# Optimization experiments

Measured on AMD Instinct MI355X. Metric: run time of the kernel, lower is better.

## Reference

```python
import jax, jax.numpy as jnp
import numpy as np

BN_EPS = 1e-5

def _l2norm(x, axis):
    return x / (1e-6 + jnp.linalg.norm(x, axis=axis, keepdims=True))

def setup_inputs() -> dict:
    key = jax.random.key(0)
    ks = jax.random.split(key, 4)
    c, k = 512, 64
    b, h, w = 16, 64, 64
    x = jax.random.normal(ks[0], (b, c, h, w), dtype=jnp.float32)
    conv1_w = jax.random.normal(ks[1], (c, c), dtype=jnp.float32) * np.sqrt(2.0 / c)
    conv1_b = jnp.zeros((c,), dtype=jnp.float32)
    mu = jax.random.normal(ks[2], (1, c, k), dtype=jnp.float32) * np.sqrt(2.0 / k)
    mu = _l2norm(mu, axis=1)
    conv2_w = jax.random.normal(ks[3], (c, c), dtype=jnp.float32) * np.sqrt(2.0 / c)
    bn_gamma = jnp.ones((c,), dtype=jnp.float32)
    bn_beta = jnp.zeros((c,), dtype=jnp.float32)
    bn_mean = jnp.zeros((c,), dtype=jnp.float32)
    bn_var = jnp.ones((c,), dtype=jnp.float32)
    return {"x": x, "conv1_w": conv1_w, "conv1_b": conv1_b, "mu": mu,
            "conv2_w": conv2_w, "bn_gamma": bn_gamma, "bn_beta": bn_beta,
            "bn_mean": bn_mean, "bn_var": bn_var}

STAGE_NUM = 3

def reference(x, conv1_w, conv1_b, mu, conv2_w, bn_gamma, bn_beta, bn_mean, bn_var):
    idn = x
    b, c, h, w = x.shape
    # conv1: 1x1 conv with bias
    xf = jnp.einsum('oc,bchw->bohw', conv1_w, x) + conv1_b[None, :, None, None]
    xf = xf.reshape(b, c, h * w)            # [b, c, n]
    mu_b = jnp.broadcast_to(mu, (b,) + mu.shape[1:])  # [b, c, k]

    # EM iterations (no-grad in original; here just the forward loop)
    def em_step(mu_b, _):
        z = jnp.einsum('bcn,bck->bnk', xf, mu_b)          # [b, n, k]
        z = jax.nn.softmax(z, axis=2)
        z_ = z / (1e-6 + z.sum(axis=1, keepdims=True))
        mu_new = _l2norm(jnp.einsum('bcn,bnk->bck', xf, z_), axis=1)
        return mu_new, z

    mu_b, zs = jax.lax.scan(em_step, mu_b, None, length=STAGE_NUM)
    z = zs[-1]                                            # last-stage responsibilities
    mu_b = jax.lax.stop_gradient(mu_b)
    z = jax.lax.stop_gradient(z)

    xr = jnp.einsum('bck,bnk->bcn', mu_b, z).reshape(b, c, h, w)
    xr = jax.nn.relu(xr)
    # conv2: 1x1 conv (no bias) + BatchNorm (inference mode)
    xr = jnp.einsum('oc,bchw->bohw', conv2_w, xr)
    inv = bn_gamma / jnp.sqrt(bn_var + BN_EPS)
    xr = xr * inv[None, :, None, None] + (bn_beta - bn_mean * inv)[None, :, None, None]
    return jax.nn.relu(xr + idn)
```

## Files before the change

kernel.cpp:

```cpp
#include <hip/hip_runtime.h>

typedef __bf16 bf16x8 __attribute__((ext_vector_type(8)));
typedef float f32x4 __attribute__((ext_vector_type(4)));

constexpr int CC = 512;
constexpr int KK = 64;
constexpr int NN = 4096;
constexpr int BB = 16;

constexpr size_t R1_OFF    = 0;
constexpr size_t R2_OFF    = 16777216;
constexpr size_t Z_OFF     = 33554432;
constexpr size_t ZT_OFF    = 35651584;
constexpr size_t MUACC_OFF = 37748736;
constexpr size_t ZSUM_OFF  = 38273024;
constexpr size_t MUBF_OFF  = 38274048;
constexpr size_t MUTBF_OFF = 38536192;
constexpr size_t W1BF_OFF  = 38798336;
constexpr size_t W2BF_OFF  = 38929408;

__global__ __launch_bounds__(256) void k_cvt(const float* __restrict__ src,
                                             __bf16* __restrict__ dst, int n8) {
    int i = blockIdx.x * 256 + threadIdx.x;
    if (i < n8) {
        const float4* s4 = (const float4*)src;
        float4 a = s4[i * 2], b = s4[i * 2 + 1];
        bf16x8 o;
        o[0] = (__bf16)a.x; o[1] = (__bf16)a.y; o[2] = (__bf16)a.z; o[3] = (__bf16)a.w;
        o[4] = (__bf16)b.x; o[5] = (__bf16)b.y; o[6] = (__bf16)b.z; o[7] = (__bf16)b.w;
        *(bf16x8*)&dst[(size_t)i * 8] = o;
    }
}

__global__ __launch_bounds__(256) void k_mu_bcast_bf(const float* __restrict__ mu_in,
                                                     __bf16* __restrict__ mu_bf,
                                                     __bf16* __restrict__ muT_bf) {
    int idx = blockIdx.x * 256 + threadIdx.x;
    if (idx < CC * KK) {
        int c = idx >> 6, k = idx & 63;
        __bf16 v = (__bf16)mu_in[idx];
        for (int b = 0; b < BB; ++b) {
            mu_bf[(size_t)b * CC * KK + idx] = v;
            muT_bf[((size_t)b * KK + k) * CC + c] = v;
        }
    }
}

__global__ __launch_bounds__(256) void k_xpose_cvt(const float* __restrict__ X,
                                                   __bf16* __restrict__ XT) {
    int n0 = blockIdx.x * 64, c0 = blockIdx.y * 64, b = blockIdx.z;
    __shared__ float T[64][65];
    int tid = threadIdx.x;
    const float* Xb = X + (size_t)b * CC * NN;
#pragma unroll
    for (int p = 0; p < 4; ++p) {
        int f4 = tid + p * 256;
        int row = f4 >> 4, col4 = (f4 & 15) * 4;
        float4 v = *(const float4*)&Xb[(size_t)(c0 + row) * NN + n0 + col4];
        T[row][col4 + 0] = v.x; T[row][col4 + 1] = v.y;
        T[row][col4 + 2] = v.z; T[row][col4 + 3] = v.w;
    }
    __syncthreads();
#pragma unroll
    for (int p = 0; p < 2; ++p) {
        int q = tid + p * 256;
        int nl = q >> 3, c8 = (q & 7) * 8;
        bf16x8 o;
#pragma unroll
        for (int j = 0; j < 8; ++j) o[j] = (__bf16)T[c8 + j][nl];
        *(bf16x8*)&XT[((size_t)b * NN + n0 + nl) * CC + c0 + c8] = o;
    }
}

__global__ __launch_bounds__(256) void k_xftrans(const __bf16* __restrict__ XFT,
                                                 __bf16* __restrict__ XFC) {
    int n0 = blockIdx.x * 64, c0 = blockIdx.y * 64, b = blockIdx.z;
    __shared__ __bf16 T[64][66];
    int tid = threadIdx.x;
#pragma unroll
    for (int p = 0; p < 2; ++p) {
        int idx = tid + p * 256;
        int row = idx >> 3, c8 = (idx & 7) * 8;
        bf16x8 v = *(const bf16x8*)&XFT[((size_t)b * NN + n0 + row) * CC + c0 + c8];
#pragma unroll
        for (int j = 0; j < 8; ++j) T[row][c8 + j] = v[j];
    }
    __syncthreads();
#pragma unroll
    for (int p = 0; p < 2; ++p) {
        int idx = tid + p * 256;
        int crow = idx >> 3, n8 = (idx & 7) * 8;
        bf16x8 o;
#pragma unroll
        for (int j = 0; j < 8; ++j) o[j] = T[n8 + j][crow];
        *(bf16x8*)&XFC[((size_t)b * CC + c0 + crow) * NN + n0 + n8] = o;
    }
}

__global__ __launch_bounds__(256) void k_conv1_mfma(
    const __bf16* __restrict__ XT, const __bf16* __restrict__ W1,
    const float* __restrict__ bias, __bf16* __restrict__ XFT) {
    __shared__ __bf16 As[2][128 * 32];
    __shared__ __bf16 Bs[2][128 * 32];
    __shared__ float sbias[128];
    int tid = threadIdx.x;
    int lane = tid & 63, wave = tid >> 6;
    int wm = wave >> 1, wn = wave & 1;
    int o0 = blockIdx.x * 128, n0 = blockIdx.y * 128, b = blockIdx.z;
    const __bf16* Ab = XT + ((size_t)b * NN + n0) * CC;
    const __bf16* Bb = W1 + (size_t)o0 * CC;
    if (tid < 128) sbias[tid] = bias[o0 + tid];

    f32x4 acc[4][4];
#pragma unroll
    for (int i = 0; i < 4; ++i)
#pragma unroll
        for (int j = 0; j < 4; ++j) acc[i][j] = f32x4{0.f, 0.f, 0.f, 0.f};

    int r0 = tid >> 2, k0c = tid & 3;
    int r1 = (tid + 256) >> 2, k1c = tid & 3;
    int w0 = r0 * 32 + (k0c ^ ((r0 >> 1) & 3)) * 8;
    int w1 = r1 * 32 + (k1c ^ ((r1 >> 1) & 3)) * 8;

    bf16x8 va0, va1, vb0, vb1;
    va0 = *(const bf16x8*)(Ab + (size_t)r0 * CC + k0c * 8);
    va1 = *(const bf16x8*)(Ab + (size_t)r1 * CC + k1c * 8);
    vb0 = *(const bf16x8*)(Bb + (size_t)r0 * CC + k0c * 8);
    vb1 = *(const bf16x8*)(Bb + (size_t)r1 * CC + k1c * 8);
    *(bf16x8*)&As[0][w0] = va0; *(bf16x8*)&As[0][w1] = va1;
    *(bf16x8*)&Bs[0][w0] = vb0; *(bf16x8*)&Bs[0][w1] = vb1;
    __syncthreads();

    for (int kt = 0; kt < 16; ++kt) {
        int s = kt & 1;
        if (kt < 15) {
            const __bf16* Ak = Ab + (kt + 1) * 32;
            const __bf16* Bk = Bb + (kt + 1) * 32;
            va0 = *(const bf16x8*)(Ak + (size_t)r0 * CC + k0c * 8);
            va1 = *(const bf16x8*)(Ak + (size_t)r1 * CC + k1c * 8);
            vb0 = *(const bf16x8*)(Bk + (size_t)r0 * CC + k0c * 8);
            vb1 = *(const bf16x8*)(Bk + (size_t)r1 * CC + k1c * 8);
        }
        bf16x8 af[4], bg[4];
#pragma unroll
        for (int f = 0; f < 4; ++f) {
            int ra = wm * 64 + f * 16 + (lane & 15);
            af[f] = *(const bf16x8*)&As[s][ra * 32 + (((lane >> 4) ^ ((ra >> 1) & 3))) * 8];
            int rb = wn * 64 + f * 16 + (lane & 15);
            bg[f] = *(const bf16x8*)&Bs[s][rb * 32 + (((lane >> 4) ^ ((rb >> 1) & 3))) * 8];
        }
#pragma unroll
        for (int i = 0; i < 4; ++i)
#pragma unroll
            for (int j = 0; j < 4; ++j)
                acc[i][j] = __builtin_amdgcn_mfma_f32_16x16x32_bf16(af[i], bg[j], acc[i][j], 0, 0, 0);
        if (kt < 15) {
            *(bf16x8*)&As[s ^ 1][w0] = va0; *(bf16x8*)&As[s ^ 1][w1] = va1;
            *(bf16x8*)&Bs[s ^ 1][w0] = vb0; *(bf16x8*)&Bs[s ^ 1][w1] = vb1;
        }
        __syncthreads();
    }

    int gq = lane >> 4, ln = lane & 15;
#pragma unroll
    for (int mf = 0; mf < 4; ++mf) {
#pragma unroll
        for (int r = 0; r < 4; ++r) {
            int n_loc = wm * 64 + mf * 16 + gq * 4 + r;
            size_t orow = ((size_t)b * NN + n0 + n_loc) * CC + o0 + wn * 64;
#pragma unroll
            for (int nf = 0; nf < 4; ++nf) {
                int o_loc = wn * 64 + nf * 16 + ln;
                XFT[orow + nf * 16 + ln] = (__bf16)(acc[mf][nf][r] + sbias[o_loc]);
            }
        }
    }
}

__global__ __launch_bounds__(256) void k_conv2_mfma(
    const __bf16* __restrict__ A, const __bf16* __restrict__ Bt,
    const float* __restrict__ gamma, const float* __restrict__ beta,
    const float* __restrict__ mean, const float* __restrict__ var,
    const float* __restrict__ Xres, float* __restrict__ Out) {
    __shared__ __bf16 As[2][128 * 32];
    __shared__ __bf16 Bs[2][128 * 32];
    __shared__ float sp0[128], sp1[128];
    int tid = threadIdx.x;
    int lane = tid & 63, wave = tid >> 6;
    int wm = wave >> 1, wn = wave & 1;
    int n0 = blockIdx.x * 128, m0 = blockIdx.y * 128, b = blockIdx.z;
    const __bf16* Ab = A + (size_t)m0 * CC;
    const __bf16* Bb = Bt + ((size_t)b * NN + n0) * CC;
    if (tid < 128) {
        float iv = gamma[m0 + tid] * rsqrtf(var[m0 + tid] + 1e-5f);
        sp0[tid] = iv;
        sp1[tid] = beta[m0 + tid] - mean[m0 + tid] * iv;
    }

    f32x4 acc[4][4];
#pragma unroll
    for (int i = 0; i < 4; ++i)
#pragma unroll
        for (int j = 0; j < 4; ++j) acc[i][j] = f32x4{0.f, 0.f, 0.f, 0.f};

    int r0 = tid >> 2, k0c = tid & 3;
    int r1 = (tid + 256) >> 2, k1c = tid & 3;
    int w0 = r0 * 32 + (k0c ^ ((r0 >> 1) & 3)) * 8;
    int w1 = r1 * 32 + (k1c ^ ((r1 >> 1) & 3)) * 8;

    bf16x8 va0, va1, vb0, vb1;
    va0 = *(const bf16x8*)(Ab + (size_t)r0 * CC + k0c * 8);
    va1 = *(const bf16x8*)(Ab + (size_t)r1 * CC + k1c * 8);
    vb0 = *(const bf16x8*)(Bb + (size_t)r0 * CC + k0c * 8);
    vb1 = *(const bf16x8*)(Bb + (size_t)r1 * CC + k1c * 8);
    *(bf16x8*)&As[0][w0] = va0; *(bf16x8*)&As[0][w1] = va1;
    *(bf16x8*)&Bs[0][w0] = vb0; *(bf16x8*)&Bs[0][w1] = vb1;
    __syncthreads();

    for (int kt = 0; kt < 16; ++kt) {
        int s = kt & 1;
        if (kt < 15) {
            const __bf16* Ak = Ab + (kt + 1) * 32;
            const __bf16* Bk = Bb + (kt + 1) * 32;
            va0 = *(const bf16x8*)(Ak + (size_t)r0 * CC + k0c * 8);
            va1 = *(const bf16x8*)(Ak + (size_t)r1 * CC + k1c * 8);
            vb0 = *(const bf16x8*)(Bk + (size_t)r0 * CC + k0c * 8);
            vb1 = *(const bf16x8*)(Bk + (size_t)r1 * CC + k1c * 8);
        }
        bf16x8 af[4], bg[4];
#pragma unroll
        for (int f = 0; f < 4; ++f) {
            int ra = wm * 64 + f * 16 + (lane & 15);
            af[f] = *(const bf16x8*)&As[s][ra * 32 + (((lane >> 4) ^ ((ra >> 1) & 3))) * 8];
            int rb = wn * 64 + f * 16 + (lane & 15);
            bg[f] = *(const bf16x8*)&Bs[s][rb * 32 + (((lane >> 4) ^ ((rb >> 1) & 3))) * 8];
        }
#pragma unroll
        for (int i = 0; i < 4; ++i)
#pragma unroll
            for (int j = 0; j < 4; ++j)
                acc[i][j] = __builtin_amdgcn_mfma_f32_16x16x32_bf16(af[i], bg[j], acc[i][j], 0, 0, 0);
        if (kt < 15) {
            *(bf16x8*)&As[s ^ 1][w0] = va0; *(bf16x8*)&As[s ^ 1][w1] = va1;
            *(bf16x8*)&Bs[s ^ 1][w0] = vb0; *(bf16x8*)&Bs[s ^ 1][w1] = vb1;
        }
        __syncthreads();
    }

    int gq = lane >> 4, ln = lane & 15;
#pragma unroll
    for (int mf = 0; mf < 4; ++mf) {
#pragma unroll
        for (int r = 0; r < 4; ++r) {
            int o_loc = wm * 64 + mf * 16 + gq * 4 + r;
            size_t orow = ((size_t)b * CC + (m0 + o_loc)) * NN + n0 + wn * 64;
#pragma unroll
            for (int nf = 0; nf < 4; ++nf) {
                int n_loc = nf * 16 + ln;
                float t = acc[mf][nf][r] * sp0[o_loc] + sp1[o_loc] + Xres[orow + n_loc];
                Out[orow + n_loc] = fmaxf(t, 0.f);
            }
        }
    }
}

__global__ __launch_bounds__(256) void k_zsoftmax_mfma(
    const __bf16* __restrict__ XFT, const __bf16* __restrict__ MUT,
    __bf16* __restrict__ Z, __bf16* __restrict__ ZT, float* __restrict__ ZSUM) {
    __shared__ __bf16 As[2][128 * 32];
    __shared__ __bf16 Bs[2][64 * 32];
    int tid = threadIdx.x;
    int lane = tid & 63, wave = tid >> 6;
    int n0 = blockIdx.x * 128, b = blockIdx.y;
    const __bf16* Ab = XFT + ((size_t)b * NN + n0) * CC;
    const __bf16* Bb = MUT + (size_t)b * KK * CC;

    f32x4 acc[2][4];
#pragma unroll
    for (int i = 0; i < 2; ++i)
#pragma unroll
        for (int j = 0; j < 4; ++j) acc[i][j] = f32x4{0.f, 0.f, 0.f, 0.f};

    int r0 = tid >> 2, k0c = tid & 3;
    int r1 = (tid + 256) >> 2, k1c = tid & 3;
    int w0 = r0 * 32 + (k0c ^ ((r0 >> 1) & 3)) * 8;
    int w1 = r1 * 32 + (k1c ^ ((r1 >> 1) & 3)) * 8;
    int rB = tid >> 2, kB = tid & 3;
    int wB = rB * 32 + (kB ^ ((rB >> 1) & 3)) * 8;

    bf16x8 va0, va1, vb0;
    va0 = *(const bf16x8*)(Ab + (size_t)r0 * CC + k0c * 8);
    va1 = *(const bf16x8*)(Ab + (size_t)r1 * CC + k1c * 8);
    vb0 = *(const bf16x8*)(Bb + (size_t)rB * CC + kB * 8);
    *(bf16x8*)&As[0][w0] = va0; *(bf16x8*)&As[0][w1] = va1;
    *(bf16x8*)&Bs[0][wB] = vb0;
    __syncthreads();

    for (int kt = 0; kt < 16; ++kt) {
        int s = kt & 1;
        if (kt < 15) {
            const __bf16* Ak = Ab + (kt + 1) * 32;
            const __bf16* Bk = Bb + (kt + 1) * 32;
            va0 = *(const bf16x8*)(Ak + (size_t)r0 * CC + k0c * 8);
            va1 = *(const bf16x8*)(Ak + (size_t)r1 * CC + k1c * 8);
            vb0 = *(const bf16x8*)(Bk + (size_t)rB * CC + kB * 8);
        }
        bf16x8 af[2], bg[4];
#pragma unroll
        for (int f = 0; f < 2; ++f) {
            int ra = wave * 32 + f * 16 + (lane & 15);
            af[f] = *(const bf16x8*)&As[s][ra * 32 + (((lane >> 4) ^ ((ra >> 1) & 3))) * 8];
        }
#pragma unroll
        for (int f = 0; f < 4; ++f) {
            int rb = f * 16 + (lane & 15);
            bg[f] = *(const bf16x8*)&Bs[s][rb * 32 + (((lane >> 4) ^ ((rb >> 1) & 3))) * 8];
        }
#pragma unroll
        for (int i = 0; i < 2; ++i)
#pragma unroll
            for (int j = 0; j < 4; ++j)
                acc[i][j] = __builtin_amdgcn_mfma_f32_16x16x32_bf16(af[i], bg[j], acc[i][j], 0, 0, 0);
        if (kt < 15) {
            *(bf16x8*)&As[s ^ 1][w0] = va0; *(bf16x8*)&As[s ^ 1][w1] = va1;
            *(bf16x8*)&Bs[s ^ 1][wB] = vb0;
        }
        __syncthreads();
    }

    int gq = lane >> 4, ln = lane & 15;
    float zp[4] = {0.f, 0.f, 0.f, 0.f};
#pragma unroll
    for (int mf = 0; mf < 2; ++mf) {
#pragma unroll
        for (int r = 0; r < 4; ++r) {
            float mx = fmaxf(fmaxf(acc[mf][0][r], acc[mf][1][r]),
                             fmaxf(acc[mf][2][r], acc[mf][3][r]));
            mx = fmaxf(mx, __shfl_xor(mx, 1));
            mx = fmaxf(mx, __shfl_xor(mx, 2));
            mx = fmaxf(mx, __shfl_xor(mx, 4));
            mx = fmaxf(mx, __shfl_xor(mx, 8));
            float e[4];
            float ssum = 0.f;
#pragma unroll
            for (int nf = 0; nf < 4; ++nf) { e[nf] = expf(acc[mf][nf][r] - mx); ssum += e[nf]; }
            ssum += __shfl_xor(ssum, 1);
            ssum += __shfl_xor(ssum, 2);
            ssum += __shfl_xor(ssum, 4);
            ssum += __shfl_xor(ssum, 8);
            float inv = 1.0f / ssum;
            int n_loc = wave * 32 + mf * 16 + gq * 4 + r;
            size_t zrow = ((size_t)b * NN + n0 + n_loc) * KK;
#pragma unroll
            for (int nf = 0; nf < 4; ++nf) {
                float zv = e[nf] * inv;
                zp[nf] += zv;
                int k = nf * 16 + ln;
                Z[zrow + k] = (__bf16)zv;
                ZT[((size_t)b * KK + k) * NN + n0 + n_loc] = (__bf16)zv;
            }
        }
    }
#pragma unroll
    for (int nf = 0; nf < 4; ++nf) {
        float t = zp[nf];
        t += __shfl_xor(t, 16);
        t += __shfl_xor(t, 32);
        if (lane < 16) atomicAdd(&ZSUM[b * KK + nf * 16 + ln], t);
    }
}

__global__ __launch_bounds__(256) void k_muacc_mfma(
    const __bf16* __restrict__ XFC, const __bf16* __restrict__ ZT,
    float* __restrict__ MUACC) {
    __shared__ __bf16 As[2][128 * 32];
    __shared__ __bf16 Bs[2][64 * 32];
    int tid = threadIdx.x;
    int lane = tid & 63, wave = tid >> 6;
    int wm = wave >> 1, wn = wave & 1;
    int c0 = (blockIdx.x & 3) * 128, sp = blockIdx.x >> 2, b = blockIdx.y;
    size_t nbase = (size_t)sp * 512;
    const __bf16* Ab = XFC + ((size_t)b * CC + c0) * NN + nbase;
    const __bf16* Bb = ZT + (size_t)b * KK * NN + nbase;

    f32x4 acc[4][2];
#pragma unroll
    for (int i = 0; i < 4; ++i)
#pragma unroll
        for (int j = 0; j < 2; ++j) acc[i][j] = f32x4{0.f, 0.f, 0.f, 0.f};

    int r0 = tid >> 2, k0c = tid & 3;
    int r1 = (tid + 256) >> 2, k1c = tid & 3;
    int w0 = r0 * 32 + (k0c ^ ((r0 >> 1) & 3)) * 8;
    int w1 = r1 * 32 + (k1c ^ ((r1 >> 1) & 3)) * 8;
    int rB = tid >> 2, kB = tid & 3;
    int wB = rB * 32 + (kB ^ ((rB >> 1) & 3)) * 8;

    bf16x8 va0, va1, vb0;
    va0 = *(const bf16x8*)(Ab + (size_t)r0 * NN + k0c * 8);
    va1 = *(const bf16x8*)(Ab + (size_t)r1 * NN + k1c * 8);
    vb0 = *(const bf16x8*)(Bb + (size_t)rB * NN + kB * 8);
    *(bf16x8*)&As[0][w0] = va0; *(bf16x8*)&As[0][w1] = va1;
    *(bf16x8*)&Bs[0][wB] = vb0;
    __syncthreads();

    for (int kt = 0; kt < 16; ++kt) {
        int s = kt & 1;
        if (kt < 15) {
            const __bf16* Ak = Ab + (kt + 1) * 32;
            const __bf16* Bk = Bb + (kt + 1) * 32;
            va0 = *(const bf16x8*)(Ak + (size_t)r0 * NN + k0c * 8);
            va1 = *(const bf16x8*)(Ak + (size_t)r1 * NN + k1c * 8);
            vb0 = *(const bf16x8*)(Bk + (size_t)rB * NN + kB * 8);
        }
        bf16x8 af[4], bg[2];
#pragma unroll
        for (int f = 0; f < 4; ++f) {
            int ra = wm * 64 + f * 16 + (lane & 15);
            af[f] = *(const bf16x8*)&As[s][ra * 32 + (((lane >> 4) ^ ((ra >> 1) & 3))) * 8];
        }
#pragma unroll
        for (int f = 0; f < 2; ++f) {
            int rb = wn * 32 + f * 16 + (lane & 15);
            bg[f] = *(const bf16x8*)&Bs[s][rb * 32 + (((lane >> 4) ^ ((rb >> 1) & 3))) * 8];
        }
#pragma unroll
        for (int i = 0; i < 4; ++i)
#pragma unroll
            for (int j = 0; j < 2; ++j)
                acc[i][j] = __builtin_amdgcn_mfma_f32_16x16x32_bf16(af[i], bg[j], acc[i][j], 0, 0, 0);
        if (kt < 15) {
            *(bf16x8*)&As[s ^ 1][w0] = va0; *(bf16x8*)&As[s ^ 1][w1] = va1;
            *(bf16x8*)&Bs[s ^ 1][wB] = vb0;
        }
        __syncthreads();
    }

    int gq = lane >> 4, ln = lane & 15;
#pragma unroll
    for (int mf = 0; mf < 4; ++mf) {
#pragma unroll
        for (int r = 0; r < 4; ++r) {
            int row = wm * 64 + mf * 16 + gq * 4 + r;
#pragma unroll
            for (int nf = 0; nf < 2; ++nf) {
                int col = wn * 32 + nf * 16 + ln;
                atomicAdd(&MUACC[((size_t)b * CC + c0 + row) * KK + col], acc[mf][nf][r]);
            }
        }
    }
}

__global__ __launch_bounds__(64) void k_munorm_bf(
    const float* __restrict__ MUACC, const float* __restrict__ ZSUM,
    __bf16* __restrict__ mu_bf, __bf16* __restrict__ muT_bf) {
    int k = blockIdx.x;
    int b = blockIdx.y;
    int lane = threadIdx.x;
    float scale = 1.0f / (1e-6f + ZSUM[b * KK + k]);
    float v[8];
    float ss = 0.f;
#pragma unroll
    for (int i = 0; i < 8; ++i) {
        v[i] = MUACC[(size_t)b * CC * KK + (size_t)(lane + i * 64) * KK + k] * scale;
        ss += v[i] * v[i];
    }
    for (int off = 32; off; off >>= 1) ss += __shfl_xor(ss, off);
    float nrm = 1.0f / (1e-6f + sqrtf(ss));
#pragma unroll
    for (int i = 0; i < 8; ++i) {
        int c = lane + i * 64;
        __bf16 o = (__bf16)(v[i] * nrm);
        mu_bf[((size_t)b * CC + c) * KK + k] = o;
        muT_bf[((size_t)b * KK + k) * CC + c] = o;
    }
}

__global__ __launch_bounds__(256) void k_xr_mfma(
    const __bf16* __restrict__ Zm, const __bf16* __restrict__ MUB,
    __bf16* __restrict__ XRT) {
    __shared__ __bf16 As[128 * 64];
    __shared__ __bf16 Bs[128 * 64];
    int tid = threadIdx.x;
    int lane = tid & 63, wave = tid >> 6;
    int wm = wave >> 1, wn = wave & 1;
    int n0 = blockIdx.x * 128, c0 = blockIdx.y * 128, b = blockIdx.z;
    const __bf16* Ab = Zm + ((size_t)b * NN + n0) * KK;
    const __bf16* Bb = MUB + ((size_t)b * CC + c0) * KK;
#pragma unroll
    for (int p = 0; p < 4; ++p) {
        int idx = tid + p * 256;
        int r = idx >> 3, ch = idx & 7;
        int woff = r * 64 + ((ch ^ (r & 7)) * 8);
        *(bf16x8*)&As[woff] = *(const bf16x8*)(Ab + (size_t)r * KK + ch * 8);
        *(bf16x8*)&Bs[woff] = *(const bf16x8*)(Bb + (size_t)r * KK + ch * 8);
    }
    __syncthreads();

    f32x4 acc[4][4];
#pragma unroll
    for (int i = 0; i < 4; ++i)
#pragma unroll
        for (int j = 0; j < 4; ++j) acc[i][j] = f32x4{0.f, 0.f, 0.f, 0.f};

    int gq = lane >> 4, ln = lane & 15;
#pragma unroll
    for (int ks = 0; ks < 2; ++ks) {
        bf16x8 af[4], bg[4];
#pragma unroll
        for (int f = 0; f < 4; ++f) {
            int ra = wm * 64 + f * 16 + ln;
            af[f] = *(const bf16x8*)&As[ra * 64 + (((ks * 4 + gq) ^ (ra & 7))) * 8];
            int rb = wn * 64 + f * 16 + ln;
            bg[f] = *(const bf16x8*)&Bs[rb * 64 + (((ks * 4 + gq) ^ (rb & 7))) * 8];
        }
#pragma unroll
        for (int i = 0; i < 4; ++i)
#pragma unroll
            for (int j = 0; j < 4; ++j)
                acc[i][j] = __builtin_amdgcn_mfma_f32_16x16x32_bf16(af[i], bg[j], acc[i][j], 0, 0, 0);
    }

#pragma unroll
    for (int mf = 0; mf < 4; ++mf) {
#pragma unroll
        for (int r = 0; r < 4; ++r) {
            int n_loc = wm * 64 + mf * 16 + gq * 4 + r;
            size_t orow = ((size_t)b * NN + n0 + n_loc) * CC + c0 + wn * 64;
#pragma unroll
            for (int nf = 0; nf < 4; ++nf) {
                XRT[orow + nf * 16 + ln] = (__bf16)fmaxf(acc[mf][nf][r], 0.f);
            }
        }
    }
}

extern "C" void kernel_launch(void* const* d_in, const int* in_sizes, int n_in,
                              void* d_out, int out_size, void* d_ws, size_t ws_size,
                              hipStream_t stream) {
    const float* x     = (const float*)d_in[0];
    const float* w1    = (const float*)d_in[1];
    const float* b1    = (const float*)d_in[2];
    const float* mu_in = (const float*)d_in[3];
    const float* w2    = (const float*)d_in[4];
    const float* gamma = (const float*)d_in[5];
    const float* beta  = (const float*)d_in[6];
    const float* mean  = (const float*)d_in[7];
    const float* var   = (const float*)d_in[8];
    float* out = (float*)d_out;
    float* ws  = (float*)d_ws;

    __bf16* xt    = (__bf16*)(ws + R1_OFF);
    __bf16* xfc   = (__bf16*)(ws + R1_OFF);
    __bf16* xft   = (__bf16*)(ws + R2_OFF);
    __bf16* xrt   = (__bf16*)(ws + R2_OFF);
    __bf16* zbf   = (__bf16*)(ws + Z_OFF);
    __bf16* ztbf  = (__bf16*)(ws + ZT_OFF);
    float*  muacc = ws + MUACC_OFF;
    float*  zsum  = ws + ZSUM_OFF;
    __bf16* mu_bf = (__bf16*)(ws + MUBF_OFF);
    __bf16* muT_bf= (__bf16*)(ws + MUTBF_OFF);
    __bf16* w1bf  = (__bf16*)(ws + W1BF_OFF);
    __bf16* w2bf  = (__bf16*)(ws + W2BF_OFF);

    hipLaunchKernelGGL(k_cvt, dim3(128), dim3(256), 0, stream, w1, w1bf, CC * CC / 8);
    hipLaunchKernelGGL(k_cvt, dim3(128), dim3(256), 0, stream, w2, w2bf, CC * CC / 8);
    hipLaunchKernelGGL(k_mu_bcast_bf, dim3(128), dim3(256), 0, stream, mu_in, mu_bf, muT_bf);
    hipLaunchKernelGGL(k_xpose_cvt, dim3(NN / 64, CC / 64, BB), dim3(256), 0, stream, x, xt);
    hipLaunchKernelGGL(k_conv1_mfma, dim3(CC / 128, NN / 128, BB), dim3(256), 0, stream,
                       xt, w1bf, b1, xft);
    hipLaunchKernelGGL(k_xftrans, dim3(NN / 64, CC / 64, BB), dim3(256), 0, stream, xft, xfc);
    for (int it = 0; it < 3; ++it) {
        hipMemsetAsync(muacc, 0, (size_t)(BB * CC * KK + BB * KK) * sizeof(float), stream);
        hipLaunchKernelGGL(k_zsoftmax_mfma, dim3(NN / 128, BB), dim3(256), 0, stream,
                           xft, muT_bf, zbf, ztbf, zsum);
        hipLaunchKernelGGL(k_muacc_mfma, dim3(32, BB), dim3(256), 0, stream, xfc, ztbf, muacc);
        hipLaunchKernelGGL(k_munorm_bf, dim3(KK, BB), dim3(64), 0, stream, muacc, zsum,
                           mu_bf, muT_bf);
    }
    hipLaunchKernelGGL(k_xr_mfma, dim3(NN / 128, CC / 128, BB), dim3(256), 0, stream,
                       zbf, mu_bf, xrt);
    hipLaunchKernelGGL(k_conv2_mfma, dim3(NN / 128, CC / 128, BB), dim3(256), 0, stream,
                       w2bf, xrt, gamma, beta, mean, var, x, out);
}
```

Baseline: 480.3 us.

## Fuse xf transpose into conv1 epilogue, stage ZT in LDS, vectorize conv2 epilogue

The separate transpose kernel that built the channel-major copy of xf is removed. The conv1 epilogue now writes both layouts directly, with 4-wide vector stores for the channel-major copy, and that copy lives in the output buffer as scratch. The softmax kernel stages z in shared memory so ZT is written with coalesced 16-byte stores, and the conv2 epilogue swaps operand roles so the residual read and output write use float4. This saves a full launch plus a read and write of xf, at the cost of strided scalar XFT stores in conv1 and extra LDS use in the softmax kernel.

```diff
diff --git a/kernel.cpp b/kernel.cpp
--- a/kernel.cpp
+++ b/kernel.cpp
@@ -1,6 +1,7 @@
 #include <hip/hip_runtime.h>
 
 typedef __bf16 bf16x8 __attribute__((ext_vector_type(8)));
+typedef __bf16 bf16x4 __attribute__((ext_vector_type(4)));
 typedef float f32x4 __attribute__((ext_vector_type(4)));
 
 constexpr int CC = 512;
@@ -72,34 +73,10 @@
     }
 }
 
-__global__ __launch_bounds__(256) void k_xftrans(const __bf16* __restrict__ XFT,
-                                                 __bf16* __restrict__ XFC) {
-    int n0 = blockIdx.x * 64, c0 = blockIdx.y * 64, b = blockIdx.z;
-    __shared__ __bf16 T[64][66];
-    int tid = threadIdx.x;
-#pragma unroll
-    for (int p = 0; p < 2; ++p) {
-        int idx = tid + p * 256;
-        int row = idx >> 3, c8 = (idx & 7) * 8;
-        bf16x8 v = *(const bf16x8*)&XFT[((size_t)b * NN + n0 + row) * CC + c0 + c8];
-#pragma unroll
-        for (int j = 0; j < 8; ++j) T[row][c8 + j] = v[j];
-    }
-    __syncthreads();
-#pragma unroll
-    for (int p = 0; p < 2; ++p) {
-        int idx = tid + p * 256;
-        int crow = idx >> 3, n8 = (idx & 7) * 8;
-        bf16x8 o;
-#pragma unroll
-        for (int j = 0; j < 8; ++j) o[j] = T[n8 + j][crow];
-        *(bf16x8*)&XFC[((size_t)b * CC + c0 + crow) * NN + n0 + n8] = o;
-    }
-}
-
 __global__ __launch_bounds__(256) void k_conv1_mfma(
     const __bf16* __restrict__ XT, const __bf16* __restrict__ W1,
-    const float* __restrict__ bias, __bf16* __restrict__ XFT) {
+    const float* __restrict__ bias, __bf16* __restrict__ XFT,
+    __bf16* __restrict__ XFC) {
     __shared__ __bf16 As[2][128 * 32];
     __shared__ __bf16 Bs[2][128 * 32];
     __shared__ float sbias[128];
@@ -165,20 +142,24 @@
 #pragma unroll
     for (int mf = 0; mf < 4; ++mf) {
 #pragma unroll
-        for (int r = 0; r < 4; ++r) {
-            int n_loc = wm * 64 + mf * 16 + gq * 4 + r;
-            size_t orow = ((size_t)b * NN + n0 + n_loc) * CC + o0 + wn * 64;
-#pragma unroll
-            for (int nf = 0; nf < 4; ++nf) {
-                int o_loc = wn * 64 + nf * 16 + ln;
-                XFT[orow + nf * 16 + ln] = (__bf16)(acc[mf][nf][r] + sbias[o_loc]);
+        for (int nf = 0; nf < 4; ++nf) {
+            int o_loc = wn * 64 + nf * 16 + ln;
+            int n_loc4 = wm * 64 + mf * 16 + gq * 4;
+            float bi = sbias[o_loc];
+            bf16x4 oc;
+#pragma unroll
+            for (int r = 0; r < 4; ++r) oc[r] = (__bf16)(acc[mf][nf][r] + bi);
+            *(bf16x4*)&XFC[((size_t)b * CC + o0 + o_loc) * NN + n0 + n_loc4] = oc;
+#pragma unroll
+            for (int r = 0; r < 4; ++r) {
+                XFT[((size_t)b * NN + n0 + n_loc4 + r) * CC + o0 + o_loc] = oc[r];
             }
         }
     }
 }
 
 __global__ __launch_bounds__(256) void k_conv2_mfma(
-    const __bf16* __restrict__ A, const __bf16* __restrict__ Bt,
+    const __bf16* __restrict__ W2, const __bf16* __restrict__ XRT,
     const float* __restrict__ gamma, const float* __restrict__ beta,
     const float* __restrict__ mean, const float* __restrict__ var,
     const float* __restrict__ Xres, float* __restrict__ Out) {
@@ -189,8 +170,8 @@
     int lane = tid & 63, wave = tid >> 6;
     int wm = wave >> 1, wn = wave & 1;
     int n0 = blockIdx.x * 128, m0 = blockIdx.y * 128, b = blockIdx.z;
-    const __bf16* Ab = A + (size_t)m0 * CC;
-    const __bf16* Bb = Bt + ((size_t)b * NN + n0) * CC;
+    const __bf16* Ab = XRT + ((size_t)b * NN + n0) * CC;
+    const __bf16* Bb = W2 + (size_t)m0 * CC;
     if (tid < 128) {
         float iv = gamma[m0 + tid] * rsqrtf(var[m0 + tid] + 1e-5f);
         sp0[tid] = iv;
@@ -251,15 +232,18 @@
 #pragma unroll
     for (int mf = 0; mf < 4; ++mf) {
 #pragma unroll
-        for (int r = 0; r < 4; ++r) {
-            int o_loc = wm * 64 + mf * 16 + gq * 4 + r;
-            size_t orow = ((size_t)b * CC + (m0 + o_loc)) * NN + n0 + wn * 64;
-#pragma unroll
-            for (int nf = 0; nf < 4; ++nf) {
-                int n_loc = nf * 16 + ln;
-                float t = acc[mf][nf][r] * sp0[o_loc] + sp1[o_loc] + Xres[orow + n_loc];
-                Out[orow + n_loc] = fmaxf(t, 0.f);
-            }
+        for (int nf = 0; nf < 4; ++nf) {
+            int o_loc = wn * 64 + nf * 16 + ln;
+            int n_loc4 = wm * 64 + mf * 16 + gq * 4;
+            size_t addr = ((size_t)b * CC + m0 + o_loc) * NN + n0 + n_loc4;
+            float iv = sp0[o_loc], sh = sp1[o_loc];
+            float4 xi = *(const float4*)&Xres[addr];
+            float4 v;
+            v.x = fmaxf(acc[mf][nf][0] * iv + sh + xi.x, 0.f);
+            v.y = fmaxf(acc[mf][nf][1] * iv + sh + xi.y, 0.f);
+            v.z = fmaxf(acc[mf][nf][2] * iv + sh + xi.z, 0.f);
+            v.w = fmaxf(acc[mf][nf][3] * iv + sh + xi.w, 0.f);
+            *(float4*)&Out[addr] = v;
         }
     }
 }
@@ -269,6 +253,7 @@
     __bf16* __restrict__ Z, __bf16* __restrict__ ZT, float* __restrict__ ZSUM) {
     __shared__ __bf16 As[2][128 * 32];
     __shared__ __bf16 Bs[2][64 * 32];
+    __shared__ __bf16 ZL[64][136];
     int tid = threadIdx.x;
     int lane = tid & 63, wave = tid >> 6;
     int n0 = blockIdx.x * 128, b = blockIdx.y;
@@ -356,8 +341,9 @@
                 float zv = e[nf] * inv;
                 zp[nf] += zv;
                 int k = nf * 16 + ln;
-                Z[zrow + k] = (__bf16)zv;
-                ZT[((size_t)b * KK + k) * NN + n0 + n_loc] = (__bf16)zv;
+                __bf16 zb = (__bf16)zv;
+                Z[zrow + k] = zb;
+                ZL[k][n_loc] = zb;
             }
         }
     }
@@ -367,6 +353,14 @@
         t += __shfl_xor(t, 16);
         t += __shfl_xor(t, 32);
         if (lane < 16) atomicAdd(&ZSUM[b * KK + nf * 16 + ln], t);
+    }
+    __syncthreads();
+#pragma unroll
+    for (int p = 0; p < 4; ++p) {
+        int ci = tid + p * 256;
+        int kr = ci >> 4, ch = (ci & 15) * 8;
+        bf16x8 v = *(const bf16x8*)&ZL[kr][ch];
+        *(bf16x8*)&ZT[((size_t)b * KK + kr) * NN + n0 + ch] = v;
     }
 }
 
@@ -551,9 +545,9 @@
     float* ws  = (float*)d_ws;
 
     __bf16* xt    = (__bf16*)(ws + R1_OFF);
-    __bf16* xfc   = (__bf16*)(ws + R1_OFF);
     __bf16* xft   = (__bf16*)(ws + R2_OFF);
     __bf16* xrt   = (__bf16*)(ws + R2_OFF);
+    __bf16* xfc   = (__bf16*)d_out;
     __bf16* zbf   = (__bf16*)(ws + Z_OFF);
     __bf16* ztbf  = (__bf16*)(ws + ZT_OFF);
     float*  muacc = ws + MUACC_OFF;
@@ -568,8 +562,7 @@
     hipLaunchKernelGGL(k_mu_bcast_bf, dim3(128), dim3(256), 0, stream, mu_in, mu_bf, muT_bf);
     hipLaunchKernelGGL(k_xpose_cvt, dim3(NN / 64, CC / 64, BB), dim3(256), 0, stream, x, xt);
     hipLaunchKernelGGL(k_conv1_mfma, dim3(CC / 128, NN / 128, BB), dim3(256), 0, stream,
-                       xt, w1bf, b1, xft);
-    hipLaunchKernelGGL(k_xftrans, dim3(NN / 64, CC / 64, BB), dim3(256), 0, stream, xft, xfc);
+                       xt, w1bf, b1, xft, xfc);
     for (int it = 0; it < 3; ++it) {
         hipMemsetAsync(muacc, 0, (size_t)(BB * CC * KK + BB * KK) * sizeof(float), stream);
         hipLaunchKernelGGL(k_zsoftmax_mfma, dim3(NN / 128, BB), dim3(256), 0, stream,
```

Result: faster. 446.2 us (-7.1%).
